# Kernel tuning notes

Measured on AMD Instinct MI355X. Metric: run time of the kernel, lower is better.

Reference implementation:

```python
import jax, jax.numpy as jnp
import numpy as np

N_STEPS = 100
TAU_S = 5.0  # network_config['tau_s']
SHAPE = (16, 128, 16, 16, N_STEPS)  # [B, C, H, W, T]


def psp(target):
    """Leaky-integrator postsynaptic potential: syn_t = syn_{t-1}*(1-1/tau_s) + x_t, emit syn_t/tau_s."""
    x = jnp.moveaxis(target, -1, 0)  # time-major [T, B, C, H, W]
    decay = 1.0 - 1.0 / TAU_S

    def step(syn, xt):
        syn = syn * decay + xt
        return syn, syn / TAU_S

    _, syns = jax.lax.scan(step, jnp.zeros_like(x[0]), x)
    return jnp.moveaxis(syns, 0, -1)  # back to [B, C, H, W, T]


def setup_inputs() -> dict:
    key = jax.random.key(0)
    k1, k2 = jax.random.split(key)
    outputs = jax.random.normal(k1, SHAPE, dtype=jnp.float32) * 0.1
    target = (jax.random.uniform(k2, SHAPE) < 0.2).astype(jnp.float32)
    return {"outputs": outputs, "target": target}


def reference(outputs, target):
    # SpikeLoss.spike_kernel: 0.5 * sum((outputs - psp(target))**2)
    delta = outputs - psp(target)
    return 0.5 * jnp.sum(delta ** 2)
```

## Files before the change

kernel.cpp:

```cpp
#include <hip/hip_runtime.h>


#define T_STEPS 100
#define N_NEURONS (16 * 128 * 16 * 16)
#define BLOCK 256
#define GRID (N_NEURONS / BLOCK)

__global__ __launch_bounds__(BLOCK) void spike_loss_partial(
    const float* __restrict__ outputs,
    const float* __restrict__ target,
    float* __restrict__ partial) {
  const int n = blockIdx.x * BLOCK + threadIdx.x;
  const float4* __restrict__ t4 =
      reinterpret_cast<const float4*>(target + (size_t)n * T_STEPS);
  const float4* __restrict__ o4 =
      reinterpret_cast<const float4*>(outputs + (size_t)n * T_STEPS);

  const float decay = 0.8f;
  const float inv_tau = 0.2f;

  float syn = 0.0f;
  float acc = 0.0f;

#pragma unroll
  for (int j = 0; j < T_STEPS / 4; ++j) {
    float4 x = t4[j];
    float4 o = o4[j];
    float d;
    syn = fmaf(syn, decay, x.x); d = fmaf(syn, -inv_tau, o.x); acc = fmaf(d, d, acc);
    syn = fmaf(syn, decay, x.y); d = fmaf(syn, -inv_tau, o.y); acc = fmaf(d, d, acc);
    syn = fmaf(syn, decay, x.z); d = fmaf(syn, -inv_tau, o.z); acc = fmaf(d, d, acc);
    syn = fmaf(syn, decay, x.w); d = fmaf(syn, -inv_tau, o.w); acc = fmaf(d, d, acc);
  }

#pragma unroll
  for (int off = 32; off > 0; off >>= 1) acc += __shfl_down(acc, off, 64);

  __shared__ float wsum[BLOCK / 64];
  const int lane = threadIdx.x & 63;
  const int wid = threadIdx.x >> 6;
  if (lane == 0) wsum[wid] = acc;
  __syncthreads();
  if (threadIdx.x == 0) {
    partial[blockIdx.x] = wsum[0] + wsum[1] + wsum[2] + wsum[3];
  }
}

__global__ __launch_bounds__(256) void spike_loss_final(
    const float* __restrict__ partial, float* __restrict__ out, int nparts) {
  float acc = 0.0f;
  for (int i = threadIdx.x; i < nparts; i += 256) acc += partial[i];
#pragma unroll
  for (int off = 32; off > 0; off >>= 1) acc += __shfl_down(acc, off, 64);
  __shared__ float wsum[4];
  const int lane = threadIdx.x & 63;
  const int wid = threadIdx.x >> 6;
  if (lane == 0) wsum[wid] = acc;
  __syncthreads();
  if (threadIdx.x == 0) out[0] = 0.5f * (wsum[0] + wsum[1] + wsum[2] + wsum[3]);
}

__global__ __launch_bounds__(BLOCK) void spike_loss_atomic(
    const float* __restrict__ outputs,
    const float* __restrict__ target,
    float* __restrict__ out) {
  const int n = blockIdx.x * BLOCK + threadIdx.x;
  const float4* __restrict__ t4 =
      reinterpret_cast<const float4*>(target + (size_t)n * T_STEPS);
  const float4* __restrict__ o4 =
      reinterpret_cast<const float4*>(outputs + (size_t)n * T_STEPS);
  const float decay = 0.8f, inv_tau = 0.2f;
  float syn = 0.0f, acc = 0.0f;
#pragma unroll
  for (int j = 0; j < T_STEPS / 4; ++j) {
    float4 x = t4[j];
    float4 o = o4[j];
    float d;
    syn = fmaf(syn, decay, x.x); d = fmaf(syn, -inv_tau, o.x); acc = fmaf(d, d, acc);
    syn = fmaf(syn, decay, x.y); d = fmaf(syn, -inv_tau, o.y); acc = fmaf(d, d, acc);
    syn = fmaf(syn, decay, x.z); d = fmaf(syn, -inv_tau, o.z); acc = fmaf(d, d, acc);
    syn = fmaf(syn, decay, x.w); d = fmaf(syn, -inv_tau, o.w); acc = fmaf(d, d, acc);
  }
#pragma unroll
  for (int off = 32; off > 0; off >>= 1) acc += __shfl_down(acc, off, 64);
  __shared__ float wsum[BLOCK / 64];
  const int lane = threadIdx.x & 63, wid = threadIdx.x >> 6;
  if (lane == 0) wsum[wid] = acc;
  __syncthreads();
  if (threadIdx.x == 0)
    atomicAdd(out, 0.5f * (wsum[0] + wsum[1] + wsum[2] + wsum[3]));
}

extern "C" void kernel_launch(void* const* d_in, const int* in_sizes, int n_in,
                              void* d_out, int out_size, void* d_ws, size_t ws_size,
                              hipStream_t stream) {
  const float* outputs = (const float*)d_in[0];
  const float* target = (const float*)d_in[1];
  float* out = (float*)d_out;

  if (ws_size >= GRID * sizeof(float)) {
    float* partial = (float*)d_ws;
    spike_loss_partial<<<GRID, BLOCK, 0, stream>>>(outputs, target, partial);
    spike_loss_final<<<1, 256, 0, stream>>>(partial, out, GRID);
  } else {
    hipMemsetAsync(out, 0, sizeof(float), stream);
    spike_loss_atomic<<<GRID, BLOCK, 0, stream>>>(outputs, target, out);
  }
}
```

Baseline: 476.3 us.

## Parallelize PSP recurrence across time with wave-level scan for coalesced loads

Each wave now handles whole neuron rows, and each of 50 lanes loads two consecutive timesteps as a float2. The leaky-integrator recurrence is computed with a shuffle-based parallel prefix scan over time, using precomputed powers of the decay. This replaces the per-thread strided float4 loads, which were poorly coalesced, with contiguous row loads. In exchange it idles 14 of 64 lanes, adds shuffle overhead, and the scan reassociates floating-point sums, so results can differ slightly.

```diff
diff --git a/kernel.cpp b/kernel.cpp
--- a/kernel.cpp
+++ b/kernel.cpp
@@ -4,46 +4,59 @@
 #define T_STEPS 100
 #define N_NEURONS (16 * 128 * 16 * 16)
 #define BLOCK 256
-#define GRID (N_NEURONS / BLOCK)
+#define GRID_P 2048
+#define NEUR_PER_WAVE (N_NEURONS / (GRID_P * BLOCK / 64))
+
+__device__ __forceinline__ float wave_scan_psp(float X, int lane) {
+  float y;
+  y = __shfl_up(X, 1);  if (lane >= 1)  X = fmaf(y, 0.64f, X);
+  y = __shfl_up(X, 2);  if (lane >= 2)  X = fmaf(y, 0.4096f, X);
+  y = __shfl_up(X, 4);  if (lane >= 4)  X = fmaf(y, 0.16777216f, X);
+  y = __shfl_up(X, 8);  if (lane >= 8)  X = fmaf(y, 2.81474977e-2f, X);
+  y = __shfl_up(X, 16); if (lane >= 16) X = fmaf(y, 7.92281625e-4f, X);
+  y = __shfl_up(X, 32); if (lane >= 32) X = fmaf(y, 6.27710174e-7f, X);
+  return X;
+}
 
 __global__ __launch_bounds__(BLOCK) void spike_loss_partial(
     const float* __restrict__ outputs,
     const float* __restrict__ target,
     float* __restrict__ partial) {
-  const int n = blockIdx.x * BLOCK + threadIdx.x;
-  const float4* __restrict__ t4 =
-      reinterpret_cast<const float4*>(target + (size_t)n * T_STEPS);
-  const float4* __restrict__ o4 =
-      reinterpret_cast<const float4*>(outputs + (size_t)n * T_STEPS);
+  const int lane = threadIdx.x & 63;
+  const int wave = (blockIdx.x * BLOCK + threadIdx.x) >> 6;
+  const bool active = lane < 50;
 
-  const float decay = 0.8f;
-  const float inv_tau = 0.2f;
+  float acc = 0.0f;
+  size_t n0 = (size_t)wave * NEUR_PER_WAVE;
 
-  float syn = 0.0f;
-  float acc = 0.0f;
+#pragma unroll 2
+  for (int i = 0; i < NEUR_PER_WAVE; ++i) {
+    const float* row_t = target + (n0 + i) * T_STEPS;
+    const float* row_o = outputs + (n0 + i) * T_STEPS;
+    float2 x = active ? reinterpret_cast<const float2*>(row_t)[lane]
+                      : make_float2(0.f, 0.f);
+    float2 o = active ? reinterpret_cast<const float2*>(row_o)[lane]
+                      : make_float2(0.f, 0.f);
 
-#pragma unroll
-  for (int j = 0; j < T_STEPS / 4; ++j) {
-    float4 x = t4[j];
-    float4 o = o4[j];
-    float d;
-    syn = fmaf(syn, decay, x.x); d = fmaf(syn, -inv_tau, o.x); acc = fmaf(d, d, acc);
-    syn = fmaf(syn, decay, x.y); d = fmaf(syn, -inv_tau, o.y); acc = fmaf(d, d, acc);
-    syn = fmaf(syn, decay, x.z); d = fmaf(syn, -inv_tau, o.z); acc = fmaf(d, d, acc);
-    syn = fmaf(syn, decay, x.w); d = fmaf(syn, -inv_tau, o.w); acc = fmaf(d, d, acc);
+    float X = fmaf(x.x, 0.8f, x.y);
+    X = wave_scan_psp(X, lane);
+    float syn1 = X;
+    float syn0 = (X - x.y) * 1.25f;
+
+    float d0 = fmaf(syn0, -0.2f, o.x);
+    float d1 = fmaf(syn1, -0.2f, o.y);
+    if (active) acc = fmaf(d0, d0, fmaf(d1, d1, acc));
   }
 
 #pragma unroll
   for (int off = 32; off > 0; off >>= 1) acc += __shfl_down(acc, off, 64);
 
   __shared__ float wsum[BLOCK / 64];
-  const int lane = threadIdx.x & 63;
   const int wid = threadIdx.x >> 6;
   if (lane == 0) wsum[wid] = acc;
   __syncthreads();
-  if (threadIdx.x == 0) {
+  if (threadIdx.x == 0)
     partial[blockIdx.x] = wsum[0] + wsum[1] + wsum[2] + wsum[3];
-  }
 }
 
 __global__ __launch_bounds__(256) void spike_loss_final(
@@ -64,27 +77,31 @@
     const float* __restrict__ outputs,
     const float* __restrict__ target,
     float* __restrict__ out) {
-  const int n = blockIdx.x * BLOCK + threadIdx.x;
-  const float4* __restrict__ t4 =
-      reinterpret_cast<const float4*>(target + (size_t)n * T_STEPS);
-  const float4* __restrict__ o4 =
-      reinterpret_cast<const float4*>(outputs + (size_t)n * T_STEPS);
-  const float decay = 0.8f, inv_tau = 0.2f;
-  float syn = 0.0f, acc = 0.0f;
-#pragma unroll
-  for (int j = 0; j < T_STEPS / 4; ++j) {
-    float4 x = t4[j];
-    float4 o = o4[j];
-    float d;
-    syn = fmaf(syn, decay, x.x); d = fmaf(syn, -inv_tau, o.x); acc = fmaf(d, d, acc);
-    syn = fmaf(syn, decay, x.y); d = fmaf(syn, -inv_tau, o.y); acc = fmaf(d, d, acc);
-    syn = fmaf(syn, decay, x.z); d = fmaf(syn, -inv_tau, o.z); acc = fmaf(d, d, acc);
-    syn = fmaf(syn, decay, x.w); d = fmaf(syn, -inv_tau, o.w); acc = fmaf(d, d, acc);
+  const int lane = threadIdx.x & 63;
+  const int wave = (blockIdx.x * BLOCK + threadIdx.x) >> 6;
+  const bool active = lane < 50;
+  float acc = 0.0f;
+  size_t n0 = (size_t)wave * NEUR_PER_WAVE;
+#pragma unroll 2
+  for (int i = 0; i < NEUR_PER_WAVE; ++i) {
+    const float* row_t = target + (n0 + i) * T_STEPS;
+    const float* row_o = outputs + (n0 + i) * T_STEPS;
+    float2 x = active ? reinterpret_cast<const float2*>(row_t)[lane]
+                      : make_float2(0.f, 0.f);
+    float2 o = active ? reinterpret_cast<const float2*>(row_o)[lane]
+                      : make_float2(0.f, 0.f);
+    float X = fmaf(x.x, 0.8f, x.y);
+    X = wave_scan_psp(X, lane);
+    float syn1 = X;
+    float syn0 = (X - x.y) * 1.25f;
+    float d0 = fmaf(syn0, -0.2f, o.x);
+    float d1 = fmaf(syn1, -0.2f, o.y);
+    if (active) acc = fmaf(d0, d0, fmaf(d1, d1, acc));
   }
 #pragma unroll
   for (int off = 32; off > 0; off >>= 1) acc += __shfl_down(acc, off, 64);
   __shared__ float wsum[BLOCK / 64];
-  const int lane = threadIdx.x & 63, wid = threadIdx.x >> 6;
+  const int wid = threadIdx.x >> 6;
   if (lane == 0) wsum[wid] = acc;
   __syncthreads();
   if (threadIdx.x == 0)
@@ -98,12 +115,12 @@
   const float* target = (const float*)d_in[1];
   float* out = (float*)d_out;
 
-  if (ws_size >= GRID * sizeof(float)) {
+  if (ws_size >= GRID_P * sizeof(float)) {
     float* partial = (float*)d_ws;
-    spike_loss_partial<<<GRID, BLOCK, 0, stream>>>(outputs, target, partial);
-    spike_loss_final<<<1, 256, 0, stream>>>(partial, out, GRID);
+    spike_loss_partial<<<GRID_P, BLOCK, 0, stream>>>(outputs, target, partial);
+    spike_loss_final<<<1, 256, 0, stream>>>(partial, out, GRID_P);
   } else {
     hipMemsetAsync(out, 0, sizeof(float), stream);
-    spike_loss_atomic<<<GRID, BLOCK, 0, stream>>>(outputs, target, out);
+    spike_loss_atomic<<<GRID_P, BLOCK, 0, stream>>>(outputs, target, out);
   }
 }
```

Measured after the change: 414.6 us. -13.0%, faster.

## Stage neuron rows through LDS and split the time scan into four segments

Applied to the files above, without the earlier changes.

Each block now loads a contiguous chunk of 64 neurons × 100 steps with fully coalesced float4 loads into shared memory, instead of each thread striding through its own 400-byte row. The 100-step recurrence is split into four 25-step segments per neuron. Segment end states are combined through precomputed decay powers (0.8^25, 0.8^50) to form each segment's carry-in, which gives four times as many threads and shorter serial chains. The cost is 25.6KB of LDS per block, extra barriers, and a small floating-point reassociation.

```diff
diff --git a/kernel.cpp b/kernel.cpp
--- a/kernel.cpp
+++ b/kernel.cpp
@@ -2,48 +2,93 @@
 
 
 #define T_STEPS 100
+#define SEG 25
+#define NPB 64
+#define BLOCK 256
 #define N_NEURONS (16 * 128 * 16 * 16)
-#define BLOCK 256
-#define GRID (N_NEURONS / BLOCK)
+#define GRID_P (N_NEURONS / NPB)
+#define F4_PER_CHUNK (NPB * T_STEPS / 4)
 
-__global__ __launch_bounds__(BLOCK) void spike_loss_partial(
-    const float* __restrict__ outputs,
-    const float* __restrict__ target,
-    float* __restrict__ partial) {
-  const int n = blockIdx.x * BLOCK + threadIdx.x;
-  const float4* __restrict__ t4 =
-      reinterpret_cast<const float4*>(target + (size_t)n * T_STEPS);
-  const float4* __restrict__ o4 =
-      reinterpret_cast<const float4*>(outputs + (size_t)n * T_STEPS);
+__device__ __forceinline__ float block_loss(const float* __restrict__ outputs,
+                                            const float* __restrict__ target) {
+  __shared__ float lbuf[NPB * T_STEPS];
+  __shared__ float lE[NPB * 4];
+  __shared__ float wsum[BLOCK / 64];
 
-  const float decay = 0.8f;
-  const float inv_tau = 0.2f;
+  const int tid = threadIdx.x;
+  const size_t base = (size_t)blockIdx.x * (NPB * T_STEPS);
+  const float4* gt = reinterpret_cast<const float4*>(target + base);
+  const float4* go = reinterpret_cast<const float4*>(outputs + base);
+  float4* lb4 = reinterpret_cast<float4*>(lbuf);
 
-  float syn = 0.0f;
-  float acc = 0.0f;
+  float4 bt[6];
+#pragma unroll
+  for (int k = 0; k < 6; ++k) bt[k] = gt[tid + 256 * k];
+  float4 tt = make_float4(0.f, 0.f, 0.f, 0.f);
+  if (tid < F4_PER_CHUNK - 1536) tt = gt[1536 + tid];
+#pragma unroll
+  for (int k = 0; k < 6; ++k) lb4[tid + 256 * k] = bt[k];
+  if (tid < F4_PER_CHUNK - 1536) lb4[1536 + tid] = tt;
+
+  float4 bo[6];
+#pragma unroll
+  for (int k = 0; k < 6; ++k) bo[k] = go[tid + 256 * k];
+  float4 to = make_float4(0.f, 0.f, 0.f, 0.f);
+  if (tid < F4_PER_CHUNK - 1536) to = go[1536 + tid];
+
+  __syncthreads();
+
+  const int n = tid >> 2;
+  const int s = tid & 3;
+  const float* xrow = lbuf + n * T_STEPS + s * SEG;
+  float x[SEG];
+#pragma unroll
+  for (int j = 0; j < SEG; ++j) x[j] = xrow[j];
+  float E = 0.f;
+#pragma unroll
+  for (int j = 0; j < SEG; ++j) E = fmaf(E, 0.8f, x[j]);
+  lE[tid] = E;
+
+  __syncthreads();
 
 #pragma unroll
-  for (int j = 0; j < T_STEPS / 4; ++j) {
-    float4 x = t4[j];
-    float4 o = o4[j];
-    float d;
-    syn = fmaf(syn, decay, x.x); d = fmaf(syn, -inv_tau, o.x); acc = fmaf(d, d, acc);
-    syn = fmaf(syn, decay, x.y); d = fmaf(syn, -inv_tau, o.y); acc = fmaf(d, d, acc);
-    syn = fmaf(syn, decay, x.z); d = fmaf(syn, -inv_tau, o.z); acc = fmaf(d, d, acc);
-    syn = fmaf(syn, decay, x.w); d = fmaf(syn, -inv_tau, o.w); acc = fmaf(d, d, acc);
+  for (int k = 0; k < 6; ++k) lb4[tid + 256 * k] = bo[k];
+  if (tid < F4_PER_CHUNK - 1536) lb4[1536 + tid] = to;
+
+  const float A25 = 3.77789319e-3f;
+  const float A50 = 1.42724769e-5f;
+  float carry = 0.f;
+  if (s >= 1) carry = lE[tid - 1];
+  if (s >= 2) carry = fmaf(A25, lE[tid - 2], carry);
+  if (s >= 3) carry = fmaf(A50, lE[tid - 3], carry);
+
+  __syncthreads();
+
+  const float* orow = lbuf + n * T_STEPS + s * SEG;
+  float syn = carry;
+  float acc = 0.f;
+#pragma unroll
+  for (int j = 0; j < SEG; ++j) {
+    syn = fmaf(syn, 0.8f, x[j]);
+    float d = fmaf(-0.2f, syn, orow[j]);
+    acc = fmaf(d, d, acc);
   }
 
 #pragma unroll
   for (int off = 32; off > 0; off >>= 1) acc += __shfl_down(acc, off, 64);
-
-  __shared__ float wsum[BLOCK / 64];
-  const int lane = threadIdx.x & 63;
-  const int wid = threadIdx.x >> 6;
+  const int lane = tid & 63;
+  const int wid = tid >> 6;
   if (lane == 0) wsum[wid] = acc;
   __syncthreads();
-  if (threadIdx.x == 0) {
-    partial[blockIdx.x] = wsum[0] + wsum[1] + wsum[2] + wsum[3];
-  }
+  return wsum[0] + wsum[1] + wsum[2] + wsum[3];
+}
+
+__global__ __launch_bounds__(BLOCK, 4) void spike_loss_partial(
+    const float* __restrict__ outputs,
+    const float* __restrict__ target,
+    float* __restrict__ partial) {
+  float blocksum = block_loss(outputs, target);
+  if (threadIdx.x == 0) partial[blockIdx.x] = blocksum;
 }
 
 __global__ __launch_bounds__(256) void spike_loss_final(
@@ -60,35 +105,12 @@
   if (threadIdx.x == 0) out[0] = 0.5f * (wsum[0] + wsum[1] + wsum[2] + wsum[3]);
 }
 
-__global__ __launch_bounds__(BLOCK) void spike_loss_atomic(
+__global__ __launch_bounds__(BLOCK, 4) void spike_loss_atomic(
     const float* __restrict__ outputs,
     const float* __restrict__ target,
     float* __restrict__ out) {
-  const int n = blockIdx.x * BLOCK + threadIdx.x;
-  const float4* __restrict__ t4 =
-      reinterpret_cast<const float4*>(target + (size_t)n * T_STEPS);
-  const float4* __restrict__ o4 =
-      reinterpret_cast<const float4*>(outputs + (size_t)n * T_STEPS);
-  const float decay = 0.8f, inv_tau = 0.2f;
-  float syn = 0.0f, acc = 0.0f;
-#pragma unroll
-  for (int j = 0; j < T_STEPS / 4; ++j) {
-    float4 x = t4[j];
-    float4 o = o4[j];
-    float d;
-    syn = fmaf(syn, decay, x.x); d = fmaf(syn, -inv_tau, o.x); acc = fmaf(d, d, acc);
-    syn = fmaf(syn, decay, x.y); d = fmaf(syn, -inv_tau, o.y); acc = fmaf(d, d, acc);
-    syn = fmaf(syn, decay, x.z); d = fmaf(syn, -inv_tau, o.z); acc = fmaf(d, d, acc);
-    syn = fmaf(syn, decay, x.w); d = fmaf(syn, -inv_tau, o.w); acc = fmaf(d, d, acc);
-  }
-#pragma unroll
-  for (int off = 32; off > 0; off >>= 1) acc += __shfl_down(acc, off, 64);
-  __shared__ float wsum[BLOCK / 64];
-  const int lane = threadIdx.x & 63, wid = threadIdx.x >> 6;
-  if (lane == 0) wsum[wid] = acc;
-  __syncthreads();
-  if (threadIdx.x == 0)
-    atomicAdd(out, 0.5f * (wsum[0] + wsum[1] + wsum[2] + wsum[3]));
+  float blocksum = block_loss(outputs, target);
+  if (threadIdx.x == 0) atomicAdd(out, 0.5f * blocksum);
 }
 
 extern "C" void kernel_launch(void* const* d_in, const int* in_sizes, int n_in,
@@ -98,12 +120,12 @@
   const float* target = (const float*)d_in[1];
   float* out = (float*)d_out;
 
-  if (ws_size >= GRID * sizeof(float)) {
+  if (ws_size >= GRID_P * sizeof(float)) {
     float* partial = (float*)d_ws;
-    spike_loss_partial<<<GRID, BLOCK, 0, stream>>>(outputs, target, partial);
-    spike_loss_final<<<1, 256, 0, stream>>>(partial, out, GRID);
+    spike_loss_partial<<<GRID_P, BLOCK, 0, stream>>>(outputs, target, partial);
+    spike_loss_final<<<1, 256, 0, stream>>>(partial, out, GRID_P);
   } else {
     hipMemsetAsync(out, 0, sizeof(float), stream);
-    spike_loss_atomic<<<GRID, BLOCK, 0, stream>>>(outputs, target, out);
+    spike_loss_atomic<<<GRID_P, BLOCK, 0, stream>>>(outputs, target, out);
   }
 }
```

New measurement: 433.4 us. 9.0% less time.
